# Kernel tuning notes

Hardware: AMD Instinct MI355X
Metric: run time of the kernel (lower is better)

## Reference

```python
import jax, jax.numpy as jnp
import numpy as np
import math

B, T, D, H = 4, 1024, 1024, 16
DK = D // H
TAU_THRESH = 0.3


def setup_inputs() -> dict:
    key = jax.random.key(0)
    ks = jax.random.split(key, 13)
    s = 1.0 / math.sqrt(D)
    return {
        "x": jax.random.normal(ks[0], (B, T, D), dtype=jnp.float32),
        "Wq": jax.random.normal(ks[1], (D, D), dtype=jnp.float32) * s,
        "bq": jax.random.normal(ks[2], (D,), dtype=jnp.float32) * s,
        "Wk": jax.random.normal(ks[3], (D, D), dtype=jnp.float32) * s,
        "bk": jax.random.normal(ks[4], (D,), dtype=jnp.float32) * s,
        "Wv": jax.random.normal(ks[5], (D, D), dtype=jnp.float32) * s,
        "bv": jax.random.normal(ks[6], (D,), dtype=jnp.float32) * s,
        "Wo": jax.random.normal(ks[7], (D, D), dtype=jnp.float32) * s,
        "bo": jax.random.normal(ks[8], (D,), dtype=jnp.float32) * s,
        "Wg1": jax.random.normal(ks[9], (1, D), dtype=jnp.float32) * s,
        "bg1": jax.random.normal(ks[10], (1,), dtype=jnp.float32) * s,
        "Wg2": jax.random.normal(ks[11], (1, D), dtype=jnp.float32) * s,
        "bg2": jax.random.normal(ks[12], (1,), dtype=jnp.float32) * s,
    }


def reference(x, Wq, bq, Wk, bk, Wv, bv, Wo, bo, Wg1, bg1, Wg2, bg2):
    b, t, d = x.shape
    # projections (torch Linear: y = x @ W.T + b)
    Q = (x @ Wq.T + bq).reshape(b, t, H, DK).transpose(0, 2, 1, 3)  # [B,H,T,dk]
    K = (x @ Wk.T + bk).reshape(b, t, H, DK).transpose(0, 2, 1, 3)
    V = (x @ Wv.T + bv).reshape(b, t, H, DK).transpose(0, 2, 1, 3)
    scores = jnp.einsum("bhqd,bhkd->bhqk", Q, K) / math.sqrt(DK)  # [B,H,T,T]
    # confidence gates from first-token query context [B, H*dk] = [B, D]
    context = Q[:, :, 0, :].reshape(b, d)
    q1 = jax.nn.sigmoid(context @ Wg1.T + bg1)  # [B,1]
    q2 = jax.nn.sigmoid(context @ Wg2.T + bg2)  # [B,1]
    c = jnp.clip(q1 * q2, 1e-8, 1.0)            # [B,1]
    tau = jnp.where(c < TAU_THRESH, 1.0 / c, jnp.ones_like(c)).reshape(b, 1, 1, 1)
    p = jax.nn.softmax(scores / tau, axis=-1)
    cb = c.reshape(b, 1, 1, 1)
    p_gated = cb * p + (1.0 - cb) * (1.0 / t)
    u = jnp.mean(1.0 - c, axis=-1, keepdims=True)  # [B,1]
    attn_out = jnp.einsum("bhqk,bhkd->bhqd", p_gated, V)
    attn_out = attn_out.transpose(0, 2, 1, 3).reshape(b, t, d)
    output = attn_out @ Wo.T + bo
    return output, u
```

## Files before the change

kernel.cpp:

```cpp
#include <hip/hip_runtime.h>
#include <stdint.h>

typedef short bf16x8 __attribute__((ext_vector_type(8)));
typedef float f32x4 __attribute__((ext_vector_type(4)));

#define MFMA_BF16(a, b, c) __builtin_amdgcn_mfma_f32_16x16x32_bf16((a), (b), (c), 0, 0, 0)

__device__ __forceinline__ short f2bf(float x) {
  union { float f; uint32_t u; } v; v.f = x;
  uint32_t r = (v.u + 0x7FFFu + ((v.u >> 16) & 1u)) >> 16;
  return (short)r;
}
__device__ __forceinline__ uint32_t rnd_bf_hi(float x) {
  union { float f; uint32_t u; } v; v.f = x;
  return v.u + 0x7FFFu + ((v.u >> 16) & 1u);
}
__device__ __forceinline__ uint32_t pack2bf(float a, float b) {
  return __builtin_amdgcn_perm(rnd_bf_hi(b), rnd_bf_hi(a), 0x07060302);
}
__device__ __forceinline__ float bfbits2f(uint32_t b16) {
  union { uint32_t u; float f; } v; v.u = b16 << 16; return v.f;
}
__device__ __forceinline__ float fexp2(float x) {
#if __has_builtin(__builtin_amdgcn_exp2f)
  return __builtin_amdgcn_exp2f(x);
#else
  return __expf(x * 0.6931471805599453f);
#endif
}
__device__ __forceinline__ void async16(const void* g, void* l) {
  __builtin_amdgcn_global_load_lds(
      (const __attribute__((address_space(1))) uint32_t*)g,
      (__attribute__((address_space(3))) uint32_t*)l, 16, 0, 0);
}

#define BAR() __builtin_amdgcn_s_barrier()
#define LGKM0() asm volatile("s_waitcnt lgkmcnt(0)" ::: "memory")
#define VMCNT(n) asm volatile("s_waitcnt vmcnt(" #n ")" ::: "memory")
#define PRIO1() __builtin_amdgcn_s_setprio(1)
#define PRIO0() __builtin_amdgcn_s_setprio(0)

__global__ __launch_bounds__(256) void prep_k(
    const float* __restrict__ x, const float* __restrict__ Wq,
    const float* __restrict__ Wk, const float* __restrict__ Wv,
    const float* __restrict__ Wo, const float* __restrict__ bq,
    short* __restrict__ xb, short* __restrict__ Wqb, short* __restrict__ Wkb,
    short* __restrict__ Wvb, short* __restrict__ Wob, float* __restrict__ ctx) {
  __shared__ float xs[1024];
  const int bid = blockIdx.x;
  const int tid = threadIdx.x;
  if (bid < 8192) {
    const float* src; short* dst; int idx;
    if (bid < 4096) {
      src = x; dst = xb; idx = (bid << 8) + tid;
    } else {
      const int r = bid - 4096;
      const int z = r >> 10;
      src = (z == 0) ? Wq : (z == 1) ? Wk : (z == 2) ? Wv : Wo;
      dst = (z == 0) ? Wqb : (z == 1) ? Wkb : (z == 2) ? Wvb : Wob;
      idx = ((r & 1023) << 8) + tid;
    }
    float4 v = ((const float4*)src)[idx];
    short4 o;
    o.x = f2bf(v.x); o.y = f2bf(v.y); o.z = f2bf(v.z); o.w = f2bf(v.w);
    ((short4*)dst)[idx] = o;
  } else {
    const int r = bid - 8192;
    const int b = r >> 4;
    const int n0 = (r & 15) << 6;
    for (int i = tid; i < 1024; i += 256) xs[i] = x[b * 1048576 + i];
    __syncthreads();
    const int w = tid >> 6, lane = tid & 63;
    const float4* xv4 = (const float4*)xs;
    for (int rr = 0; rr < 16; ++rr) {
      const int n = n0 + (w << 4) + rr;
      const float4* wrow = (const float4*)(Wq + n * 1024);
      float p = 0.f;
#pragma unroll
      for (int c2 = 0; c2 < 4; ++c2) {
        float4 wv = wrow[lane + (c2 << 6)];
        float4 xv = xv4[lane + (c2 << 6)];
        p += xv.x * wv.x + xv.y * wv.y + xv.z * wv.z + xv.w * wv.w;
      }
#pragma unroll
      for (int off = 32; off; off >>= 1) p += __shfl_xor(p, off);
      if (lane == 0) ctx[b * 1024 + n] = p + bq[n];
    }
  }
}

__global__ __launch_bounds__(256) void gates_fin(const float* __restrict__ ctx,
                                                 const float* __restrict__ Wg1,
                                                 const float* __restrict__ bg1,
                                                 const float* __restrict__ Wg2,
                                                 const float* __restrict__ bg2,
                                                 float* __restrict__ gates,
                                                 float* __restrict__ u_out) {
  __shared__ float red[16];
  const int tid = threadIdx.x, w = tid >> 6, lane = tid & 63;
  for (int b = 0; b < 4; ++b) {
    float4 cv = ((const float4*)(ctx + b * 1024))[tid];
    float4 w1 = ((const float4*)Wg1)[tid];
    float4 w2 = ((const float4*)Wg2)[tid];
    float p1 = cv.x * w1.x + cv.y * w1.y + cv.z * w1.z + cv.w * w1.w;
    float p2 = cv.x * w2.x + cv.y * w2.y + cv.z * w2.z + cv.w * w2.w;
#pragma unroll
    for (int off = 32; off; off >>= 1) { p1 += __shfl_xor(p1, off); p2 += __shfl_xor(p2, off); }
    if (lane == 0) { red[w] = p1; red[8 + w] = p2; }
    __syncthreads();
    if (tid == 0) {
      float g1 = red[0] + red[1] + red[2] + red[3] + bg1[0];
      float g2 = red[8] + red[9] + red[10] + red[11] + bg2[0];
      float q1 = 1.f / (1.f + expf(-g1));
      float q2 = 1.f / (1.f + expf(-g2));
      float c = fminf(fmaxf(q1 * q2, 1e-8f), 1.0f);
      gates[b * 2 + 0] = c;
      gates[b * 2 + 1] = (c < 0.3f ? c : 1.0f) * 0.125f * 1.4426950408889634f;
      u_out[b] = 1.0f - c;
    }
    __syncthreads();
  }
}

template <bool SWP>
__device__ __forceinline__ void qkv_core(const short* __restrict__ xb,
                                         const short* __restrict__ W,
                                         const float* __restrict__ bias,
                                         short* __restrict__ out,
                                         short* sm, int m0, int nl0) {
  const int tid = threadIdx.x;
  const int wid = tid >> 6, lane = tid & 63;
  const int wr = wid >> 2, wc = wid & 3;
  const int m15 = lane & 15, quad = lane >> 4;
  const int swz = m15 & 7;

  const int rowb = tid >> 3;
  const int cs = ((tid & 7) ^ (rowb & 7)) << 3;
  const short* aB = xb + (m0 + rowb) * 1024 + cs;
  const short* bB = W + (nl0 + rowb) * 1024 + cs;

  short* As = sm;
  short* Bs = sm + 32768;

#define STAGEH(sb, tt, hf, dst)                        \
  do {                                                 \
    const short* _s = (sb) + (hf)*131072 + (tt)*64;    \
    short* _d = (dst) + ((hf) << 13) + (tid << 3);     \
    async16(_s, _d);                                   \
    async16(_s + 65536, _d + 4096);                    \
  } while (0)

#define RD(base, f, kk)                                                        \
  (*(const bf16x8*)((base) + ((f) << 10) + (m15 << 6) +                        \
                    (((((kk) << 2) + quad) ^ swz) << 3)))

#define MM(accr, af, bf)                                   \
  do {                                                     \
    if (SWP) accr = MFMA_BF16((bf), (af), (accr));         \
    else     accr = MFMA_BF16((af), (bf), (accr));         \
  } while (0)

  f32x4 acc[8][4];
#pragma unroll
  for (int i = 0; i < 8; ++i)
#pragma unroll
    for (int j = 0; j < 4; ++j) { f32x4 zz = {0.f, 0.f, 0.f, 0.f}; acc[i][j] = zz; }

  STAGEH(bB, 0, 0, Bs);
  STAGEH(aB, 0, 0, As);
  STAGEH(aB, 0, 1, As);
  STAGEH(bB, 0, 1, Bs);
  STAGEH(bB, 1, 0, Bs + 16384);
  STAGEH(aB, 1, 0, As + 16384);
  VMCNT(4);
  BAR();

  bf16x8 a[4][2], b0[2][2], b1[2][2];

  for (int t = 0; t < 16; ++t) {
    const int buf = t & 1;
    const short* Ab = As + (buf << 14) + (wr << 13);
    const short* Bb = Bs + (buf << 14) + ((wc >> 1) << 13) + ((wc & 1) << 12);
    short* Adn = As + ((buf ^ 1) << 14);
    short* Bdn = Bs + ((buf ^ 1) << 14);
    short* Ad2 = As + (buf << 14);
    short* Bd2 = Bs + (buf << 14);

#pragma unroll
    for (int fi = 0; fi < 4; ++fi) { a[fi][0] = RD(Ab, fi, 0); a[fi][1] = RD(Ab, fi, 1); }
#pragma unroll
    for (int fj = 0; fj < 2; ++fj) { b0[fj][0] = RD(Bb, fj, 0); b0[fj][1] = RD(Bb, fj, 1); }
    if (t < 15) STAGEH(aB, t + 1, 1, Adn);
    BAR();
    LGKM0();
    PRIO1();
#pragma unroll
    for (int fi = 0; fi < 4; ++fi)
#pragma unroll
      for (int fj = 0; fj < 2; ++fj) {
        MM(acc[fi][fj], a[fi][0], b0[fj][0]);
        MM(acc[fi][fj], a[fi][1], b0[fj][1]);
      }
    PRIO0();
    BAR();

#pragma unroll
    for (int fj = 0; fj < 2; ++fj) { b1[fj][0] = RD(Bb, 2 + fj, 0); b1[fj][1] = RD(Bb, 2 + fj, 1); }
    if (t < 15) STAGEH(bB, t + 1, 1, Bdn);
    BAR();
    LGKM0();
    PRIO1();
#pragma unroll
    for (int fi = 0; fi < 4; ++fi)
#pragma unroll
      for (int fj = 0; fj < 2; ++fj) {
        MM(acc[fi][2 + fj], a[fi][0], b1[fj][0]);
        MM(acc[fi][2 + fj], a[fi][1], b1[fj][1]);
      }
    PRIO0();
    BAR();

#pragma unroll
    for (int fi = 0; fi < 4; ++fi) { a[fi][0] = RD(Ab, 4 + fi, 0); a[fi][1] = RD(Ab, 4 + fi, 1); }
    if (t < 14) STAGEH(bB, t + 2, 0, Bd2);
    BAR();
    LGKM0();
    PRIO1();
#pragma unroll
    for (int fi = 0; fi < 4; ++fi)
#pragma unroll
      for (int fj = 0; fj < 2; ++fj) {
        MM(acc[4 + fi][2 + fj], a[fi][0], b1[fj][0]);
        MM(acc[4 + fi][2 + fj], a[fi][1], b1[fj][1]);
      }
    PRIO0();
    BAR();

    if (t < 14) STAGEH(aB, t + 2, 0, Ad2);
    BAR();
    PRIO1();
#pragma unroll
    for (int fi = 0; fi < 4; ++fi)
#pragma unroll
      for (int fj = 0; fj < 2; ++fj) {
        MM(acc[4 + fi][fj], a[fi][0], b0[fj][0]);
        MM(acc[4 + fi][fj], a[fi][1], b0[fj][1]);
      }
    PRIO0();
    if (t < 14) { VMCNT(4); }
    else if (t == 14) { VMCNT(0); }
    BAR();
  }

  const int nw = nl0 + (wc << 6);
  if (SWP) {
#pragma unroll
    for (int fj = 0; fj < 4; ++fj) {
      const int n = nw + (fj << 4) + (quad << 2);
      const float4 bv = *(const float4*)(bias + n);
      const int hh = n >> 6, dk0 = n & 63;
#pragma unroll
      for (int fi = 0; fi < 8; ++fi) {
        const int m = m0 + (wr << 7) + (fi << 4) + m15;
        const int bb = m >> 10, tt = m & 1023;
        uint2 st;
        st.x = pack2bf(acc[fi][fj][0] + bv.x, acc[fi][fj][1] + bv.y);
        st.y = pack2bf(acc[fi][fj][2] + bv.z, acc[fi][fj][3] + bv.w);
        *(uint2*)(out + (((bb << 4) + hh) << 16) + (tt << 6) + dk0) = st;
      }
    }
  } else {
#pragma unroll
    for (int fj = 0; fj < 4; ++fj) {
      const int n = nw + (fj << 4) + m15;
      const float bv = bias[n];
      const int hh = n >> 6, dk = n & 63;
#pragma unroll
      for (int fi = 0; fi < 8; ++fi) {
        const int m = m0 + (wr << 7) + (fi << 4) + (quad << 2);
        const int bb = m >> 10, t0 = m & 1023;
        uint2 st;
        st.x = pack2bf(acc[fi][fj][0] + bv, acc[fi][fj][1] + bv);
        st.y = pack2bf(acc[fi][fj][2] + bv, acc[fi][fj][3] + bv);
        *(uint2*)(out + (((bb << 4) + hh) << 16) + (dk << 10) + t0) = st;
      }
    }
  }
#undef STAGEH
#undef RD
#undef MM
}

__global__ __launch_bounds__(512) void gemm_qkv8(
    const short* __restrict__ xb,
    const short* __restrict__ Wqb, const short* __restrict__ Wkb, const short* __restrict__ Wvb,
    const float* __restrict__ bq, const float* __restrict__ bk, const float* __restrict__ bv,
    short* __restrict__ Qh, short* __restrict__ Kh, short* __restrict__ Vt) {
  const int lin = blockIdx.x;
  const int s = ((lin & 7) * 24) + (lin >> 3);
  const int bx = s & 15, by = s >> 4;
  const int z = by >> 2;
  const int m0 = bx << 8, nl0 = (by & 3) << 8;
  extern __shared__ short sm[];
  if (z == 0)      qkv_core<true >(xb, Wqb, bq, Qh, sm, m0, nl0);
  else if (z == 1) qkv_core<true >(xb, Wkb, bk, Kh, sm, m0, nl0);
  else             qkv_core<false>(xb, Wvb, bv, Vt, sm, m0, nl0);
}

__global__ __launch_bounds__(256) void gemm_out(const short* __restrict__ Ab,
                                                const short* __restrict__ Wo,
                                                const float* __restrict__ bo,
                                                float* __restrict__ Cout) {
  const int m0 = blockIdx.x << 6;
  const int n0 = blockIdx.y << 7;
  const int tid = threadIdx.x;
  const int w = tid >> 6, lane = tid & 63;
  const int m15 = lane & 15, quad = lane >> 4;
  const int wr = w >> 1, wc = w & 1;

  __shared__ short As[2048];
  __shared__ short Bs[4096];

  f32x4 acc[2][4];
#pragma unroll
  for (int i = 0; i < 2; ++i)
#pragma unroll
    for (int j = 0; j < 4; ++j) { f32x4 zz = {0.f, 0.f, 0.f, 0.f}; acc[i][j] = zz; }

  const int s0 = tid, s1 = tid + 256;
  const int arow = s0 >> 2, alcb = (s0 & 3) ^ ((arow >> 1) & 3);
  const int brow1 = s1 >> 2, blcb1 = (s1 & 3) ^ ((brow1 >> 1) & 3);
  const short* gA  = Ab + (m0 + arow) * 1024 + (alcb << 3);
  const short* gB0 = Wo + (n0 + arow) * 1024 + (alcb << 3);
  const short* gB1 = Wo + (n0 + brow1) * 1024 + (blcb1 << 3);
  short* lA  = &As[s0 << 3];
  short* lB0 = &Bs[s0 << 3];
  short* lB1 = &Bs[s1 << 3];

  for (int kt = 0; kt < 32; ++kt) {
    async16(gA, lA);
    async16(gB0, lB0); async16(gB1, lB1);
    gA += 32; gB0 += 32; gB1 += 32;
    __syncthreads();
    bf16x8 a[2], b[4];
#pragma unroll
    for (int i = 0; i < 2; ++i) {
      const int ra = (wr << 5) + (i << 4) + m15;
      a[i] = *(const bf16x8*)(&As[ra * 32 + ((quad ^ ((ra >> 1) & 3)) << 3)]);
    }
#pragma unroll
    for (int j = 0; j < 4; ++j) {
      const int rb = (wc << 6) + (j << 4) + m15;
      b[j] = *(const bf16x8*)(&Bs[rb * 32 + ((quad ^ ((rb >> 1) & 3)) << 3)]);
    }
#pragma unroll
    for (int i = 0; i < 2; ++i)
#pragma unroll
      for (int j = 0; j < 4; ++j)
        acc[i][j] = MFMA_BF16(a[i], b[j], acc[i][j]);
    __syncthreads();
  }

#pragma unroll
  for (int j = 0; j < 4; ++j) {
    const int n = n0 + (wc << 6) + (j << 4) + m15;
    const float bb_ = bo[n];
#pragma unroll
    for (int i = 0; i < 2; ++i) {
      const int mb = m0 + (wr << 5) + (i << 4) + (quad << 2);
#pragma unroll
      for (int r = 0; r < 4; ++r)
        Cout[(mb + r) * 1024 + n] = acc[i][j][r] + bb_;
    }
  }
}

__global__ __launch_bounds__(256) void meanv_k(const short* __restrict__ Vt,
                                               float* __restrict__ mV) {
  const int bh = blockIdx.x;
  const int tid = threadIdx.x;
  const int d = tid >> 2, part = tid & 3;
  const short* row = Vt + bh * 65536 + d * 1024 + part * 256;
  float s = 0.f;
#pragma unroll 4
  for (int i = 0; i < 64; ++i) {
    uint2 v = *(const uint2*)(row + i * 4);
    s += bfbits2f(v.x & 0xffffu) + bfbits2f(v.x >> 16) +
         bfbits2f(v.y & 0xffffu) + bfbits2f(v.y >> 16);
  }
  s += __shfl_xor(s, 1);
  s += __shfl_xor(s, 2);
  if (part == 0) mV[bh * 64 + d] = s;
}

__global__ __launch_bounds__(256, 4) void attn_k(const short* __restrict__ Qh,
                                                 const short* __restrict__ Kh,
                                                 const short* __restrict__ Vt,
                                                 const float* __restrict__ gates,
                                                 const float* __restrict__ mV,
                                                 short* __restrict__ attnb) {
  const int bh = blockIdx.x;
  const int b = bh >> 4, h = bh & 15;
  const int q0 = blockIdx.y << 6;
  const int tid = threadIdx.x;
  const int w = tid >> 6, lane = tid & 63;
  const int m15 = lane & 15, quad = lane >> 4;

  __shared__ short Ks[2][4096];
  __shared__ short Vs[2][4096];

  const short* ksrc = Kh + bh * 65536;
  const short* vsrc = Vt + bh * 65536;

  const float sl = gates[b * 2 + 1];

  const short* qsrc = Qh + ((bh << 10) + q0 + (w << 4) + m15) * 64;
  const bf16x8 qb0 = *(const bf16x8*)(qsrc + (quad << 3));
  const bf16x8 qb1 = *(const bf16x8*)(qsrc + 32 + (quad << 3));

  const int off0 = tid, off1 = tid + 256;
  const int r0 = off0 >> 3, cb0 = (off0 & 7) ^ (r0 & 7);
  const int r1 = off1 >> 3, cb1 = (off1 & 7) ^ (r1 & 7);

#define STAGE(kv, bufi)                                                        \
  do {                                                                         \
    async16(ksrc + (((kv) << 6) + r0) * 64 + (cb0 << 3), &Ks[bufi][off0 << 3]);\
    async16(ksrc + (((kv) << 6) + r1) * 64 + (cb1 << 3), &Ks[bufi][off1 << 3]);\
    async16(vsrc + r0 * 1024 + ((kv) << 6) + (cb0 << 3), &Vs[bufi][off0 << 3]);\
    async16(vsrc + r1 * 1024 + ((kv) << 6) + (cb1 << 3), &Vs[bufi][off1 << 3]);\
  } while (0)

  STAGE(0, 0);

  float lsum = 0.f;
  f32x4 o_acc[4];
#pragma unroll
  for (int jd = 0; jd < 4; ++jd) { f32x4 zz = {0.f, 0.f, 0.f, 0.f}; o_acc[jd] = zz; }

  const int srcA = ((quad & 1) << 5) + m15;
  const int srcB = srcA + 16;
  const bool selhi = (quad & 2) != 0;

  for (int kv = 0; kv < 16; ++kv) {
    __syncthreads();
    if (kv < 15) STAGE(kv + 1, (kv + 1) & 1);
    const short* Kb = &Ks[kv & 1][0];
    const short* Vb = &Vs[kv & 1][0];

    f32x4 sacc[4];
#pragma unroll
    for (int s = 0; s < 4; ++s) {
      const int row = (s << 4) + m15;
      const int sw = row & 7;
      bf16x8 a0 = *(const bf16x8*)(Kb + (row << 6) + ((quad ^ sw) << 3));
      bf16x8 a1 = *(const bf16x8*)(Kb + (row << 6) + (((quad + 4) ^ sw) << 3));
      f32x4 zz = {0.f, 0.f, 0.f, 0.f};
      zz = MFMA_BF16(a0, qb0, zz);
      zz = MFMA_BF16(a1, qb1, zz);
      sacc[s] = zz;
    }

    uint32_t pk[4][2];
#pragma unroll
    for (int s = 0; s < 4; ++s) {
      float p0 = fexp2(sacc[s][0] * sl);
      float p1 = fexp2(sacc[s][1] * sl);
      float p2 = fexp2(sacc[s][2] * sl);
      float p3 = fexp2(sacc[s][3] * sl);
      lsum += (p0 + p1) + (p2 + p3);
      pk[s][0] = pack2bf(p0, p1);
      pk[s][1] = pack2bf(p2, p3);
    }

    bf16x8 pf[2];
#pragma unroll
    for (int H = 0; H < 2; ++H) {
      uint32_t f[4];
#pragma unroll
      for (int rp = 0; rp < 2; ++rp) {
        uint32_t alo = (uint32_t)__shfl((int)pk[2 * H][rp], srcA);
        uint32_t ahi = (uint32_t)__shfl((int)pk[2 * H + 1][rp], srcA);
        uint32_t blo = (uint32_t)__shfl((int)pk[2 * H][rp], srcB);
        uint32_t bhi = (uint32_t)__shfl((int)pk[2 * H + 1][rp], srcB);
        f[rp]     = selhi ? ahi : alo;
        f[2 + rp] = selhi ? bhi : blo;
      }
      pf[H] = *(bf16x8*)f;
    }

#pragma unroll
    for (int jd = 0; jd < 4; ++jd) {
      const int row = (jd << 4) + m15;
      const int sw = row & 7;
      bf16x8 v0 = *(const bf16x8*)(Vb + (row << 6) + ((quad ^ sw) << 3));
      bf16x8 v1 = *(const bf16x8*)(Vb + (row << 6) + (((quad + 4) ^ sw) << 3));
      o_acc[jd] = MFMA_BF16(v0, pf[0], o_acc[jd]);
      o_acc[jd] = MFMA_BF16(v1, pf[1], o_acc[jd]);
    }
  }
#undef STAGE

  float l = lsum;
  l += __shfl_xor(l, 16);
  l += __shfl_xor(l, 32);

  const float cg = gates[b * 2 + 0];
  const float s0 = cg / l;
  const float coef = (1.0f - cg) * (1.0f / 1024.0f);
  const int qrow = q0 + (w << 4) + m15;
  short* orow = attnb + ((b << 10) + qrow) * 1024 + (h << 6);
#pragma unroll
  for (int jd = 0; jd < 4; ++jd) {
    float4 mv = *(const float4*)(mV + (bh << 6) + (jd << 4) + (quad << 2));
    float v0_ = s0 * o_acc[jd][0] + coef * mv.x;
    float v1_ = s0 * o_acc[jd][1] + coef * mv.y;
    float v2_ = s0 * o_acc[jd][2] + coef * mv.z;
    float v3_ = s0 * o_acc[jd][3] + coef * mv.w;
    uint2 st;
    st.x = pack2bf(v0_, v1_);
    st.y = pack2bf(v2_, v3_);
    *(uint2*)(orow + (jd << 4) + (quad << 2)) = st;
  }
}

extern "C" void kernel_launch(void* const* d_in, const int* in_sizes, int n_in,
                              void* d_out, int out_size, void* d_ws, size_t ws_size,
                              hipStream_t stream) {
  const float* x   = (const float*)d_in[0];
  const float* Wq  = (const float*)d_in[1];
  const float* bq  = (const float*)d_in[2];
  const float* Wk  = (const float*)d_in[3];
  const float* bk  = (const float*)d_in[4];
  const float* Wv  = (const float*)d_in[5];
  const float* bv  = (const float*)d_in[6];
  const float* Wo  = (const float*)d_in[7];
  const float* bo  = (const float*)d_in[8];
  const float* Wg1 = (const float*)d_in[9];
  const float* bg1 = (const float*)d_in[10];
  const float* Wg2 = (const float*)d_in[11];
  const float* bg2 = (const float*)d_in[12];
  float* out = (float*)d_out;

  char* ws = (char*)d_ws;
  short* xb   = (short*)(ws + 0);
  short* Wqb  = (short*)(ws + 8388608);
  short* Wkb  = (short*)(ws + 10485760);
  short* Wvb  = (short*)(ws + 12582912);
  short* Wob  = (short*)(ws + 14680064);
  short* Qh   = (short*)(ws + 16777216);
  short* Kh   = (short*)(ws + 25165824);
  short* Vt   = (short*)(ws + 33554432);
  short* attb = (short*)(ws + 41943040);
  float* ctx  = (float*)(ws + 50331648);
  float* gat  = (float*)(ws + 50348032);
  float* mV   = (float*)(ws + 50348064);

  static bool lds_inited = false;
  if (!lds_inited) {
    hipFuncSetAttribute(reinterpret_cast<const void*>(gemm_qkv8),
                        hipFuncAttributeMaxDynamicSharedMemorySize, 131072);
    lds_inited = true;
  }

  prep_k<<<8256, 256, 0, stream>>>(x, Wq, Wk, Wv, Wo, bq,
                                   xb, Wqb, Wkb, Wvb, Wob, ctx);
  gates_fin<<<1, 256, 0, stream>>>(ctx, Wg1, bg1, Wg2, bg2, gat, out + 4194304);

  gemm_qkv8<<<192, 512, 131072, stream>>>(xb, Wqb, Wkb, Wvb, bq, bk, bv,
                                          Qh, Kh, Vt);
  meanv_k<<<64, 256, 0, stream>>>(Vt, mV);
  attn_k<<<dim3(64, 16), 256, 0, stream>>>(Qh, Kh, Vt, gat, mV, attb);
  gemm_out<<<dim3(64, 8), 256, 0, stream>>>(attb, Wob, bo, out);
}
```

Baseline: 213.2 us.

## Process two 64-row query tiles per attention block to reuse staged K/V

Each attention block now handles 128 query rows instead of 64: every wave holds two sets of Q fragments and accumulators, and each K/V tile staged into shared memory is used for both. This halves global K/V traffic and the number of staging and sync rounds per query row, and doubles MFMA work between barriers. In exchange register pressure roughly doubles (launch bounds drop from 4 to 2 blocks per SM) and the grid shrinks to 512 blocks, which lowers occupancy and latency hiding.

After: 211.7 us. Within noise of the previous version (-0.7%).

```diff
diff --git a/kernel.cpp b/kernel.cpp
--- a/kernel.cpp
+++ b/kernel.cpp
@@ -393,7 +393,7 @@
   if (part == 0) mV[bh * 64 + d] = s;
 }
 
-__global__ __launch_bounds__(256, 4) void attn_k(const short* __restrict__ Qh,
+__global__ __launch_bounds__(256, 2) void attn_k(const short* __restrict__ Qh,
                                                  const short* __restrict__ Kh,
                                                  const short* __restrict__ Vt,
                                                  const float* __restrict__ gates,
@@ -401,7 +401,7 @@
                                                  short* __restrict__ attnb) {
   const int bh = blockIdx.x;
   const int b = bh >> 4, h = bh & 15;
-  const int q0 = blockIdx.y << 6;
+  const int q0 = blockIdx.y << 7;
   const int tid = threadIdx.x;
   const int w = tid >> 6, lane = tid & 63;
   const int m15 = lane & 15, quad = lane >> 4;
@@ -414,9 +414,12 @@
 
   const float sl = gates[b * 2 + 1];
 
-  const short* qsrc = Qh + ((bh << 10) + q0 + (w << 4) + m15) * 64;
-  const bf16x8 qb0 = *(const bf16x8*)(qsrc + (quad << 3));
-  const bf16x8 qb1 = *(const bf16x8*)(qsrc + 32 + (quad << 3));
+  const short* qsrcA = Qh + ((bh << 10) + q0 + (w << 4) + m15) * 64;
+  const short* qsrcB = qsrcA + 64 * 64;
+  const bf16x8 qA0 = *(const bf16x8*)(qsrcA + (quad << 3));
+  const bf16x8 qA1 = *(const bf16x8*)(qsrcA + 32 + (quad << 3));
+  const bf16x8 qB0 = *(const bf16x8*)(qsrcB + (quad << 3));
+  const bf16x8 qB1 = *(const bf16x8*)(qsrcB + 32 + (quad << 3));
 
   const int off0 = tid, off1 = tid + 256;
   const int r0 = off0 >> 3, cb0 = (off0 & 7) ^ (r0 & 7);
@@ -432,14 +435,35 @@
 
   STAGE(0, 0);
 
-  float lsum = 0.f;
-  f32x4 o_acc[4];
-#pragma unroll
-  for (int jd = 0; jd < 4; ++jd) { f32x4 zz = {0.f, 0.f, 0.f, 0.f}; o_acc[jd] = zz; }
+  float lsumA = 0.f, lsumB = 0.f;
+  f32x4 oA[4], oB[4];
+#pragma unroll
+  for (int jd = 0; jd < 4; ++jd) {
+    f32x4 zz = {0.f, 0.f, 0.f, 0.f};
+    oA[jd] = zz; oB[jd] = zz;
+  }
 
   const int srcA = ((quad & 1) << 5) + m15;
   const int srcB = srcA + 16;
   const bool selhi = (quad & 2) != 0;
+
+#define BUILD_PF(pf, pk)                                                       \
+  do {                                                                         \
+    _Pragma("unroll")                                                          \
+    for (int Hh = 0; Hh < 2; ++Hh) {                                           \
+      uint32_t f[4];                                                           \
+      _Pragma("unroll")                                                        \
+      for (int rp = 0; rp < 2; ++rp) {                                         \
+        uint32_t alo = (uint32_t)__shfl((int)pk[2 * Hh][rp], srcA);            \
+        uint32_t ahi = (uint32_t)__shfl((int)pk[2 * Hh + 1][rp], srcA);        \
+        uint32_t blo = (uint32_t)__shfl((int)pk[2 * Hh][rp], srcB);            \
+        uint32_t bhi = (uint32_t)__shfl((int)pk[2 * Hh + 1][rp], srcB);        \
+        f[rp]     = selhi ? ahi : alo;                                         \
+        f[2 + rp] = selhi ? bhi : blo;                                         \
+      }                                                                        \
+      pf[Hh] = *(bf16x8*)f;                                                    \
+    }                                                                          \
+  } while (0)
 
   for (int kv = 0; kv < 16; ++kv) {
     __syncthreads();
@@ -447,46 +471,45 @@
     const short* Kb = &Ks[kv & 1][0];
     const short* Vb = &Vs[kv & 1][0];
 
-    f32x4 sacc[4];
+    f32x4 sA[4], sB[4];
 #pragma unroll
     for (int s = 0; s < 4; ++s) {
       const int row = (s << 4) + m15;
       const int sw = row & 7;
       bf16x8 a0 = *(const bf16x8*)(Kb + (row << 6) + ((quad ^ sw) << 3));
       bf16x8 a1 = *(const bf16x8*)(Kb + (row << 6) + (((quad + 4) ^ sw) << 3));
-      f32x4 zz = {0.f, 0.f, 0.f, 0.f};
-      zz = MFMA_BF16(a0, qb0, zz);
-      zz = MFMA_BF16(a1, qb1, zz);
-      sacc[s] = zz;
-    }
-
-    uint32_t pk[4][2];
+      f32x4 zA = {0.f, 0.f, 0.f, 0.f};
+      zA = MFMA_BF16(a0, qA0, zA);
+      zA = MFMA_BF16(a1, qA1, zA);
+      sA[s] = zA;
+      f32x4 zB = {0.f, 0.f, 0.f, 0.f};
+      zB = MFMA_BF16(a0, qB0, zB);
+      zB = MFMA_BF16(a1, qB1, zB);
+      sB[s] = zB;
+    }
+
+    uint32_t pkA[4][2], pkB[4][2];
 #pragma unroll
     for (int s = 0; s < 4; ++s) {
-      float p0 = fexp2(sacc[s][0] * sl);
-      float p1 = fexp2(sacc[s][1] * sl);
-      float p2 = fexp2(sacc[s][2] * sl);
-      float p3 = fexp2(sacc[s][3] * sl);
-      lsum += (p0 + p1) + (p2 + p3);
-      pk[s][0] = pack2bf(p0, p1);
-      pk[s][1] = pack2bf(p2, p3);
-    }
-
-    bf16x8 pf[2];
-#pragma unroll
-    for (int H = 0; H < 2; ++H) {
-      uint32_t f[4];
-#pragma unroll
-      for (int rp = 0; rp < 2; ++rp) {
-        uint32_t alo = (uint32_t)__shfl((int)pk[2 * H][rp], srcA);
-        uint32_t ahi = (uint32_t)__shfl((int)pk[2 * H + 1][rp], srcA);
-        uint32_t blo = (uint32_t)__shfl((int)pk[2 * H][rp], srcB);
-        uint32_t bhi = (uint32_t)__shfl((int)pk[2 * H + 1][rp], srcB);
-        f[rp]     = selhi ? ahi : alo;
-        f[2 + rp] = selhi ? bhi : blo;
-      }
-      pf[H] = *(bf16x8*)f;
-    }
+      float a0 = fexp2(sA[s][0] * sl);
+      float a1 = fexp2(sA[s][1] * sl);
+      float a2 = fexp2(sA[s][2] * sl);
+      float a3 = fexp2(sA[s][3] * sl);
+      lsumA += (a0 + a1) + (a2 + a3);
+      pkA[s][0] = pack2bf(a0, a1);
+      pkA[s][1] = pack2bf(a2, a3);
+      float b0 = fexp2(sB[s][0] * sl);
+      float b1 = fexp2(sB[s][1] * sl);
+      float b2 = fexp2(sB[s][2] * sl);
+      float b3 = fexp2(sB[s][3] * sl);
+      lsumB += (b0 + b1) + (b2 + b3);
+      pkB[s][0] = pack2bf(b0, b1);
+      pkB[s][1] = pack2bf(b2, b3);
+    }
+
+    bf16x8 pfA[2], pfB[2];
+    BUILD_PF(pfA, pkA);
+    BUILD_PF(pfB, pkB);
 
 #pragma unroll
     for (int jd = 0; jd < 4; ++jd) {
@@ -494,32 +517,40 @@
       const int sw = row & 7;
       bf16x8 v0 = *(const bf16x8*)(Vb + (row << 6) + ((quad ^ sw) << 3));
       bf16x8 v1 = *(const bf16x8*)(Vb + (row << 6) + (((quad + 4) ^ sw) << 3));
-      o_acc[jd] = MFMA_BF16(v0, pf[0], o_acc[jd]);
-      o_acc[jd] = MFMA_BF16(v1, pf[1], o_acc[jd]);
+      oA[jd] = MFMA_BF16(v0, pfA[0], oA[jd]);
+      oA[jd] = MFMA_BF16(v1, pfA[1], oA[jd]);
+      oB[jd] = MFMA_BF16(v0, pfB[0], oB[jd]);
+      oB[jd] = MFMA_BF16(v1, pfB[1], oB[jd]);
     }
   }
 #undef STAGE
-
-  float l = lsum;
-  l += __shfl_xor(l, 16);
-  l += __shfl_xor(l, 32);
+#undef BUILD_PF
+
+  float lA = lsumA;
+  lA += __shfl_xor(lA, 16);
+  lA += __shfl_xor(lA, 32);
+  float lB = lsumB;
+  lB += __shfl_xor(lB, 16);
+  lB += __shfl_xor(lB, 32);
 
   const float cg = gates[b * 2 + 0];
-  const float s0 = cg / l;
+  const float sc0A = cg / lA;
+  const float sc0B = cg / lB;
   const float coef = (1.0f - cg) * (1.0f / 1024.0f);
-  const int qrow = q0 + (w << 4) + m15;
-  short* orow = attnb + ((b << 10) + qrow) * 1024 + (h << 6);
+  const int qrowA = q0 + (w << 4) + m15;
+  short* orowA = attnb + ((b << 10) + qrowA) * 1024 + (h << 6);
+  short* orowB = orowA + 64 * 1024;
 #pragma unroll
   for (int jd = 0; jd < 4; ++jd) {
     float4 mv = *(const float4*)(mV + (bh << 6) + (jd << 4) + (quad << 2));
-    float v0_ = s0 * o_acc[jd][0] + coef * mv.x;
-    float v1_ = s0 * o_acc[jd][1] + coef * mv.y;
-    float v2_ = s0 * o_acc[jd][2] + coef * mv.z;
-    float v3_ = s0 * o_acc[jd][3] + coef * mv.w;
-    uint2 st;
-    st.x = pack2bf(v0_, v1_);
-    st.y = pack2bf(v2_, v3_);
-    *(uint2*)(orow + (jd << 4) + (quad << 2)) = st;
+    uint2 stA;
+    stA.x = pack2bf(sc0A * oA[jd][0] + coef * mv.x, sc0A * oA[jd][1] + coef * mv.y);
+    stA.y = pack2bf(sc0A * oA[jd][2] + coef * mv.z, sc0A * oA[jd][3] + coef * mv.w);
+    *(uint2*)(orowA + (jd << 4) + (quad << 2)) = stA;
+    uint2 stB;
+    stB.x = pack2bf(sc0B * oB[jd][0] + coef * mv.x, sc0B * oB[jd][1] + coef * mv.y);
+    stB.y = pack2bf(sc0B * oB[jd][2] + coef * mv.z, sc0B * oB[jd][3] + coef * mv.w);
+    *(uint2*)(orowB + (jd << 4) + (quad << 2)) = stB;
   }
 }
 
@@ -569,6 +600,6 @@
   gemm_qkv8<<<192, 512, 131072, stream>>>(xb, Wqb, Wkb, Wvb, bq, bk, bv,
                                           Qh, Kh, Vt);
   meanv_k<<<64, 256, 0, stream>>>(Vt, mV);
-  attn_k<<<dim3(64, 16), 256, 0, stream>>>(Qh, Kh, Vt, gat, mV, attb);
+  attn_k<<<dim3(64, 8), 256, 0, stream>>>(Qh, Kh, Vt, gat, mV, attb);
   gemm_out<<<dim3(64, 8), 256, 0, stream>>>(attb, Wob, bo, out);
 }
```
